# Kernel tuning notes

Measured on AMD Instinct MI355X. Metric: run time of the kernel, lower is better.

The kernel has to match this reference:

```python
import jax, jax.numpy as jnp
import numpy as np

B, T, V, E, Hd, NTAG = 16, 512, 32000, 100, 500, 32
PAD, SOS, EOS = 0, 1, 2
NEG = -10000.0


def _lstm_dir(xs, mask, Wih, Whh, b, h0, c0, reverse):
    # xs: [T,B,D]; mask: [T,B] bool. Packed-sequence semantics: at padded
    # steps the state is frozen and the output is zero (pad_packed fills 0).
    def step(carry, inp):
        h, c = carry
        x_t, m = inp
        g = x_t @ Wih.T + h @ Whh.T + b
        i, f, gg, o = jnp.split(g, 4, axis=-1)  # torch gate order i,f,g,o
        c_new = jax.nn.sigmoid(f) * c + jax.nn.sigmoid(i) * jnp.tanh(gg)
        h_new = jax.nn.sigmoid(o) * jnp.tanh(c_new)
        m_ = m[:, None]
        return (jnp.where(m_, h_new, h), jnp.where(m_, c_new, c)), jnp.where(m_, h_new, 0.0)
    _, ys = jax.lax.scan(step, (h0, c0), (xs, mask), reverse=reverse)
    return ys


def _forward(x, y0, embed_W, Wih0, Whh0, bih0, bhh0, Wih1, Whh1, bih1, bhh1, W_out, b_out, trans, h0, c0):
    maskb = x > 0                       # [B,T]
    maskf = maskb.astype(embed_W.dtype)
    mT = maskb.T                        # [T,B]
    xs = embed_W[x].transpose(1, 0, 2)  # [T,B,E]
    # layer 0 (bidirectional)
    f0 = _lstm_dir(xs, mT, Wih0[0], Whh0[0], bih0[0] + bhh0[0], h0[0], c0[0], False)
    b0 = _lstm_dir(xs, mT, Wih0[1], Whh0[1], bih0[1] + bhh0[1], h0[1], c0[1], True)
    l1 = jnp.concatenate([f0, b0], axis=-1)  # [T,B,1000]
    # layer 1 (dropout omitted: deterministic reference)
    f1 = _lstm_dir(l1, mT, Wih1[0], Whh1[0], bih1[0] + bhh1[0], h0[2], c0[2], False)
    b1 = _lstm_dir(l1, mT, Wih1[1], Whh1[1], bih1[1] + bhh1[1], h0[3], c0[3], True)
    hseq = jnp.concatenate([f1, b1], axis=-1).transpose(1, 0, 2)  # [B,T,1000]
    # emissions, masked exactly as in loss(): y = y * mask
    y = (hseq @ W_out.T + b_out) * maskf[:, :, None]  # [B,T,NTAG]
    # gold path score (crf_score_batch)
    y0e = jnp.concatenate([jnp.full((B, 1), SOS, y0.dtype), y0], axis=1)
    emit = jnp.take_along_axis(y, y0e[:, 1:, None], axis=2)[..., 0]
    tr = trans[y0e[:, 1:], y0e[:, :-1]] * maskf
    gold = jnp.sum(emit + tr, axis=1)  # [B]
    # log-partition (crf_forward_batch). Faithful to the original, including
    # the quirk that finished rows are overwritten with max_g score[b,g].
    init = jnp.full((B, NTAG), NEG, y.dtype).at[:, SOS].set(0.0)
    def step(score, inp):
        emit_t, m_t = inp  # [B,NTAG], [B]
        z = score[:, None, :] + trans[None, :, :] + emit_t[:, :, None]  # [B,F,G]
        new = jax.nn.logsumexp(z, axis=2)
        carry = jnp.broadcast_to(jnp.max(score, axis=1, keepdims=True), score.shape)
        return jnp.where(m_t[:, None], new, carry), None
    final, _ = jax.lax.scan(step, init, (y.transpose(1, 0, 2), mT))
    Z = jax.nn.logsumexp(final, axis=1)
    return jnp.mean(Z - gold)


def setup_inputs() -> dict:
    key = jax.random.key(0)
    ks = jax.random.split(key, 14)
    rng = np.random.default_rng(0)
    lengths = np.sort(rng.integers(T // 4, T + 1, size=B))[::-1]  # sorted desc (pack_padded)
    valid = np.arange(T)[None, :] < lengths[:, None]
    x = rng.integers(1, V, size=(B, T)) * valid
    y0 = rng.integers(3, NTAG, size=(B, T)) * valid
    rn = lambda k, s, sc=0.1: jax.random.normal(k, s, jnp.float32) * sc
    embed_W = rn(ks[0], (V, E)).at[0].set(0.0)  # padding_idx=0
    Wih0, Whh0 = rn(ks[1], (2, 4 * Hd, E)), rn(ks[2], (2, 4 * Hd, Hd))
    bih0, bhh0 = rn(ks[3], (2, 4 * Hd)), rn(ks[4], (2, 4 * Hd))
    Wih1, Whh1 = rn(ks[5], (2, 4 * Hd, 2 * Hd)), rn(ks[6], (2, 4 * Hd, Hd))
    bih1, bhh1 = rn(ks[7], (2, 4 * Hd)), rn(ks[8], (2, 4 * Hd))
    W_out, b_out = rn(ks[9], (NTAG, 2 * Hd)), rn(ks[10], (NTAG,))
    trans = jax.random.normal(ks[11], (NTAG, NTAG), jnp.float32)
    trans = trans.at[SOS, :].set(NEG).at[:, EOS].set(NEG).at[:, PAD].set(NEG).at[PAD, :].set(NEG)
    trans = trans.at[PAD, EOS].set(0.0).at[PAD, PAD].set(0.0)
    h0 = jax.random.normal(ks[12], (4, B, Hd), jnp.float32)
    c0 = jax.random.normal(ks[13], (4, B, Hd), jnp.float32)
    return dict(x=jnp.asarray(x, jnp.int32), y0=jnp.asarray(y0, jnp.int32), embed_W=embed_W,
                Wih0=Wih0, Whh0=Whh0, bih0=bih0, bhh0=bhh0, Wih1=Wih1, Whh1=Whh1,
                bih1=bih1, bhh1=bhh1, W_out=W_out, b_out=b_out, trans=trans, h0=h0, c0=c0)


def reference(x, y0, embed_W, Wih0, Whh0, bih0, bhh0, Wih1, Whh1, bih1, bhh1, W_out, b_out, trans, h0, c0):
    return _forward(x, y0, embed_W, Wih0, Whh0, bih0, bhh0, Wih1, Whh1, bih1, bhh1, W_out, b_out, trans, h0, c0)
```

## Files before the change

### kernel.cpp

```cpp
#include <hip/hip_runtime.h>
#include <hip/hip_fp16.h>
#include <math.h>

#define TT 512
#define BB 16
#define EE 100
#define HD 500
#define NEG (-10000.0f)
#define SENT64 0xFFFFFFFFFFFFFFFFull
#define SENT32 0xFFFFFFFFu

typedef __attribute__((ext_vector_type(8))) short short8;
typedef __attribute__((ext_vector_type(4))) float f32x4;
typedef __attribute__((ext_vector_type(4))) unsigned int u32x4;
typedef __attribute__((ext_vector_type(2))) unsigned int u32x2;

__device__ inline short f2bf(float f) {
    unsigned u = __builtin_bit_cast(unsigned, f);
    unsigned r = (u + 0x7fffu + ((u >> 16) & 1u)) >> 16;
    return (short)r;
}
__device__ inline unsigned short f2h(float f) {
    __half h = __float2half(f);
    return __builtin_bit_cast(unsigned short, h);
}
__device__ inline float h2f(unsigned short u) {
    __half h = __builtin_bit_cast(__half, u);
    return __half2float(h);
}
__device__ inline float bf2f(unsigned short u) {
    return __builtin_bit_cast(float, ((unsigned)u) << 16);
}
__device__ inline float sigm_fast(float x) {
    return __builtin_amdgcn_rcpf(1.f + __expf(-x));
}
__device__ inline float tanh_fast(float x) {
    return 1.f - 2.f * __builtin_amdgcn_rcpf(__expf(2.f * x) + 1.f);
}
__device__ inline void store_u16_wt(unsigned short* p, unsigned short v) {
    asm volatile("global_store_short %0, %1, off sc0 sc1" :: "v"(p), "v"((unsigned)v) : "memory");
}
__device__ inline void store_sent16(void* p) {
    u32x4 s = {SENT32, SENT32, SENT32, SENT32};
    asm volatile("global_store_dwordx4 %0, %1, off sc0 sc1" :: "v"(p), "v"(s) : "memory");
}

#define NSENTB   4104
#define NEMB     4096
#define NWC0     2000
#define NPAD     384
__global__ __launch_bounds__(256) void prep_kernel(
    const int* __restrict__ x, int* __restrict__ mlen,
    unsigned long long* __restrict__ sentp, int* __restrict__ gcnt,
    const float* __restrict__ EW, unsigned short* __restrict__ XS,
    const float* __restrict__ Wih0, unsigned short* __restrict__ Wb0,
    int* __restrict__ H0pad) {
    int bid = blockIdx.x;
    int tid = threadIdx.x;
    if (bid == 0) {
        __shared__ int mx;
        if (tid == 0) mx = 1;
        if (tid < 132)
            __hip_atomic_store(gcnt + tid, 0, __ATOMIC_RELAXED, __HIP_MEMORY_SCOPE_AGENT);
        __syncthreads();
        int any0 = 0, any1 = 0;
        for (int b = 0; b < BB; ++b) {
            any0 |= (x[b * TT + tid] > 0);
            any1 |= (x[b * TT + tid + 256] > 0);
        }
        if (any0) atomicMax(&mx, tid + 1);
        if (any1) atomicMax(&mx, tid + 257);
        __syncthreads();
        if (tid == 0) mlen[0] = mx;
        return;
    }
    bid -= 1;
    if (bid < NSENTB) {
        int i = bid * 256 + tid;
        store_sent16((char*)sentp + (size_t)i * 16);
        return;
    }
    bid -= NSENTB;
    if (bid < NEMB) {
        int idx = bid * 256 + tid;
        int e = idx & 127;
        int r = idx >> 7;
        int t = r >> 4;
        int b = r & 15;
        unsigned short v = 0;
        if (e < EE) {
            int tok = x[b * TT + t];
            v = (unsigned short)f2bf(EW[(size_t)tok * EE + e]);
        }
        XS[idx] = v;
        return;
    }
    bid -= NEMB;
    if (bid < NWC0) {
        int i = bid * 256 + tid;
        int r = i >> 7;
        int k = i & 127;
        int z = r / 2000;
        int rl = r - z * 2000;
        int logical = (rl & 3) * 500 + (rl >> 2);
        Wb0[i] = (k < 100)
            ? (unsigned short)f2bf(Wih0[((size_t)z * 2000 + logical) * 100 + k]) : 0;
        return;
    }
    bid -= NWC0;
    {
        int i = bid * 256 + tid;
        if (i < 8192 * 12) {
            int r = i / 12, c = i - r * 12;
            H0pad[r * 512 + 500 + c] = 0;
        }
    }
}

__global__ void sentfill_kernel(unsigned long long* __restrict__ p, int n16,
                                int* __restrict__ cnt) {
    int i = blockIdx.x * 256 + threadIdx.x;
    if (i < n16)
        store_sent16((char*)p + (size_t)i * 16);
    if (cnt && blockIdx.x == 0 && threadIdx.x < 132)
        __hip_atomic_store(cnt + threadIdx.x, 0, __ATOMIC_RELAXED, __HIP_MEMORY_SCOPE_AGENT);
}

__device__ __forceinline__ void gemm_body(
    const unsigned short* __restrict__ A, const unsigned short* __restrict__ W,
    const float* __restrict__ b1, const float* __restrict__ b2,
    unsigned short* __restrict__ C, int Kpad, int bx, int by, int z,
    int* gcnt) {
    __shared__ __align__(16) unsigned short AsS[128 * 40];
    __shared__ __align__(16) unsigned short WsS[64 * 40];
    const int tid = threadIdx.x;
    const int lane = tid & 63;
    const int w = tid >> 6;
    const int quad = lane >> 4;
    const int nl = lane & 15;
    const int bm0 = bx * 128;
    const int n0 = by * 64;

    const unsigned short* Wz = W + (size_t)z * 2000 * Kpad;
    unsigned short* Cz = C + (size_t)z * 8192 * 2000;
    const float* b1z = b1 + (size_t)z * 2000;
    const float* b2z = b2 + (size_t)z * 2000;

    f32x4 acc[2][4];
#pragma unroll
    for (int mt = 0; mt < 2; ++mt)
#pragma unroll
        for (int nt = 0; nt < 4; ++nt) acc[mt][nt] = (f32x4){0.f, 0.f, 0.f, 0.f};

    const int arow = tid >> 2;
    const int kc = tid & 3;
    const int wn = n0 + arow;
    const bool wok = (wn < 2000);

    const unsigned short* Ap0 = A + (size_t)(bm0 + arow) * Kpad + kc * 8;
    const unsigned short* Ap1 = A + (size_t)(bm0 + 64 + arow) * Kpad + kc * 8;
    const unsigned short* Wp  = Wz + (size_t)(wok ? wn : 0) * Kpad + kc * 8;

    short8 av0 = *(const short8*)(Ap0);
    short8 av1 = *(const short8*)(Ap1);
    short8 wv = {0, 0, 0, 0, 0, 0, 0, 0};
    if (wok) wv = *(const short8*)(Wp);

    for (int k0 = 0; k0 < Kpad; k0 += 32) {
        __syncthreads();
        *(short8*)&AsS[arow * 40 + kc * 8] = av0;
        *(short8*)&AsS[(64 + arow) * 40 + kc * 8] = av1;
        *(short8*)&WsS[arow * 40 + kc * 8] = wv;
        __syncthreads();

        if (k0 + 32 < Kpad) {
            av0 = *(const short8*)(Ap0 + k0 + 32);
            av1 = *(const short8*)(Ap1 + k0 + 32);
            if (wok) wv = *(const short8*)(Wp + k0 + 32);
        }

        short8 af[2], bfr[4];
#pragma unroll
        for (int mt = 0; mt < 2; ++mt)
            af[mt] = *(const short8*)&AsS[(w * 32 + mt * 16 + nl) * 40 + quad * 8];
#pragma unroll
        for (int nt = 0; nt < 4; ++nt)
            bfr[nt] = *(const short8*)&WsS[(nt * 16 + nl) * 40 + quad * 8];
#pragma unroll
        for (int mt = 0; mt < 2; ++mt)
#pragma unroll
            for (int nt = 0; nt < 4; ++nt)
                acc[mt][nt] = __builtin_amdgcn_mfma_f32_16x16x32_bf16(
                    af[mt], bfr[nt], acc[mt][nt], 0, 0, 0);
    }

#pragma unroll
    for (int nt = 0; nt < 4; ++nt) {
        int n = n0 + nt * 16 + nl;
        if (n < 2000) {
            int lg = n & 3, kk = n >> 2;
            float bb = b1z[lg * 500 + kk] + b2z[lg * 500 + kk];
#pragma unroll
            for (int mt = 0; mt < 2; ++mt) {
                int mbase = bm0 + w * 32 + mt * 16 + quad * 4;
#pragma unroll
                for (int reg = 0; reg < 4; ++reg)
                    store_u16_wt(&Cz[(size_t)(mbase + reg) * 2000 + n],
                                 f2h(acc[mt][nt][reg] + bb));
            }
        }
    }
    asm volatile("s_waitcnt vmcnt(0)" ::: "memory");
    __syncthreads();
    if (tid == 0)
        __hip_atomic_fetch_add(&gcnt[z * 64 + bx], 1,
                               __ATOMIC_RELAXED, __HIP_MEMORY_SCOPE_AGENT);
}

__device__ __forceinline__ void rec_body(
    const unsigned short* __restrict__ G, const float* __restrict__ Whh,
    const int* __restrict__ x, const float* __restrict__ h0,
    const float* __restrict__ c0, int layerbase,
    unsigned short* __restrict__ Hout, unsigned short* __restrict__ hseq,
    const int* __restrict__ mlen, int* gcnt, int blk)
{
    const int dir = blk >> 4;
    const int bsl = blk & 15;
    const int k0 = bsl * 32;
    const int tid = threadIdx.x;
    const int lane = tid & 63;
    const int w = tid >> 6;
    const int quad = lane >> 4;
    const int nl = lane & 15;
    const int L = mlen[0];

    const float* Wd = Whh + (size_t)dir * 2000 * HD;
    const unsigned short* Gd = G + (size_t)dir * TT * BB * 2000;
    unsigned short* hdir = hseq + (size_t)dir * (TT + 1) * 8192;

    __shared__ __align__(16) unsigned short hstage[8192];
    __shared__ float sg[4][32][17];

    short8 bf[2][16];
#pragma unroll
    for (int tl = 0; tl < 2; ++tl) {
        int tt = w * 2 + tl;
        int r = tt * 16 + nl;
        int g = r >> 5;
        int lkr = r & 31;
        int kk = k0 + lkr;
        const float* wrow = (kk < HD) ? (Wd + (size_t)(g * HD + kk) * HD) : (const float*)0;
#pragma unroll
        for (int ks = 0; ks < 16; ++ks) {
            int kg0 = ks * 32 + quad * 8;
            short8 v;
            if (wrow && kg0 + 8 <= HD) {
                float4 f0 = *(const float4*)(wrow + kg0);
                float4 f1 = *(const float4*)(wrow + kg0 + 4);
                v[0] = f2bf(f0.x); v[1] = f2bf(f0.y); v[2] = f2bf(f0.z); v[3] = f2bf(f0.w);
                v[4] = f2bf(f1.x); v[5] = f2bf(f1.y); v[6] = f2bf(f1.z); v[7] = f2bf(f1.w);
            } else {
#pragma unroll
                for (int j = 0; j < 8; ++j) {
                    int kg = kg0 + j;
                    float f = (wrow && kg < HD) ? wrow[kg] : 0.f;
                    v[j] = f2bf(f);
                }
            }
            bf[tl][ks] = v;
        }
    }

    const int lk = tid & 31;
    const int k  = k0 + lk;
    const bool kok = (k < HD);
    const int b0v = tid >> 5;
    const int b1v = 8 + (tid >> 5);
    float h_st[2] = {0.f, 0.f}, c_st[2] = {0.f, 0.f};
    if (kok) {
        size_t base0 = (size_t)(layerbase + dir) * BB * HD + (size_t)b0v * HD + k;
        size_t base1 = (size_t)(layerbase + dir) * BB * HD + (size_t)b1v * HD + k;
        h_st[0] = h0[base0]; c_st[0] = c0[base0];
        h_st[1] = h0[base1]; c_st[1] = c0[base1];
    }

    {
        int i0 = (int)(unsigned short)f2bf(kok ? h_st[0] : 0.f);
        int i1 = (int)(unsigned short)f2bf(kok ? h_st[1] : 0.f);
        int a0 = __shfl_down(i0, 1), c0s = __shfl_down(i0, 2), d0 = __shfl_down(i0, 3);
        int a1 = __shfl_down(i1, 1), c1s = __shfl_down(i1, 2), d1 = __shfl_down(i1, 3);
        if ((lk & 3) == 0) {
            unsigned long long p0 = (unsigned long long)(unsigned)(i0 | (a0 << 16))
                                  | ((unsigned long long)(unsigned)(c0s | (d0 << 16)) << 32);
            unsigned long long p1 = (unsigned long long)(unsigned)(i1 | (a1 << 16))
                                  | ((unsigned long long)(unsigned)(c1s | (d1 << 16)) << 32);
            int idx0 = bsl * 512 + (b0v + 16 * (lk >> 3)) * 8 + (lk & 7);
            int idx1 = bsl * 512 + (b1v + 16 * (lk >> 3)) * 8 + (lk & 7);
            __hip_atomic_store((unsigned long long*)(hdir + idx0), p0,
                               __ATOMIC_RELAXED, __HIP_MEMORY_SCOPE_AGENT);
            __hip_atomic_store((unsigned long long*)(hdir + idx1), p1,
                               __ATOMIC_RELAXED, __HIP_MEMORY_SCOPE_AGENT);
        }
    }

    u32x2 ga = {0, 0}, gb = {0, 0};
    int m[2]; m[0] = m[1] = 0;
    int lastTile = -1;

    {
        int t = dir ? (L - 1) : 0;
        if (gcnt) {
            int tile = dir * 64 + (t >> 3);
            while (__hip_atomic_load(&gcnt[tile], __ATOMIC_RELAXED,
                                     __HIP_MEMORY_SCOPE_AGENT) < 32) {}
            lastTile = tile;
        }
        if (kok) {
            const unsigned short* gr0 = Gd + ((size_t)t * BB + b0v) * 2000 + (size_t)k * 4;
            const unsigned short* gr1 = Gd + ((size_t)t * BB + b1v) * 2000 + (size_t)k * 4;
            asm volatile(
                "global_load_dwordx2 %0, %2, off sc0 sc1\n\t"
                "global_load_dwordx2 %1, %3, off sc0 sc1"
                : "=&v"(ga), "=&v"(gb) : "v"(gr0), "v"(gr1) : "memory");
            m[0] = x[b0v * TT + t] > 0;
            m[1] = x[b1v * TT + t] > 0;
        }
    }

    for (int s = 0; s < L; ++s) {
        const int t = dir ? (L - 1 - s) : s;
        const unsigned short* bufr = hdir + (size_t)s * 8192;
        unsigned short* bufw = hdir + (size_t)(s + 1) * 8192;

        {
            const unsigned short* p0 = bufr + (tid +   0) * 8;
            const unsigned short* p1 = bufr + (tid + 256) * 8;
            const unsigned short* p2 = bufr + (tid + 512) * 8;
            const unsigned short* p3 = bufr + (tid + 768) * 8;
            u32x4 c0v, c1v, c2v, c3v;
            for (;;) {
                asm volatile(
                    "global_load_dwordx4 %0, %6, off sc0 sc1\n\t"
                    "global_load_dwordx4 %1, %7, off sc0 sc1\n\t"
                    "global_load_dwordx4 %2, %8, off sc0 sc1\n\t"
                    "global_load_dwordx4 %3, %9, off sc0 sc1\n\t"
                    "s_waitcnt vmcnt(0)"
                    : "=&v"(c0v), "=&v"(c1v), "=&v"(c2v), "=&v"(c3v),
                      "+v"(ga), "+v"(gb)
                    : "v"(p0), "v"(p1), "v"(p2), "v"(p3)
                    : "memory");
                unsigned bad = 0;
#pragma unroll
                for (int q = 0; q < 4; ++q)
                    bad |= (c0v[q] == SENT32) | (c1v[q] == SENT32)
                         | (c2v[q] == SENT32) | (c3v[q] == SENT32);
                if (!bad) break;
            }
            *(u32x4*)&hstage[(tid +   0) * 8] = c0v;
            *(u32x4*)&hstage[(tid + 256) * 8] = c1v;
            *(u32x4*)&hstage[(tid + 512) * 8] = c2v;
            *(u32x4*)&hstage[(tid + 768) * 8] = c3v;
        }
        __syncthreads();

        f32x4 acc0 = {0.f, 0.f, 0.f, 0.f};
        f32x4 acc1 = {0.f, 0.f, 0.f, 0.f};
#pragma unroll
        for (int ks = 0; ks < 16; ++ks) {
            short8 a = *(const short8*)&hstage[ks * 512 + lane * 8];
            acc0 = __builtin_amdgcn_mfma_f32_16x16x32_bf16(a, bf[0][ks], acc0, 0, 0, 0);
            acc1 = __builtin_amdgcn_mfma_f32_16x16x32_bf16(a, bf[1][ks], acc1, 0, 0, 0);
        }

        {
            int r0 = (w * 2 + 0) * 16 + nl;
            int r1 = (w * 2 + 1) * 16 + nl;
            int g0r = r0 >> 5, lk0 = r0 & 31;
            int g1r = r1 >> 5, lk1 = r1 & 31;
#pragma unroll
            for (int reg = 0; reg < 4; ++reg) {
                int b = quad * 4 + reg;
                sg[g0r][lk0][b] = acc0[reg];
                sg[g1r][lk1][b] = acc1[reg];
            }
        }
        __syncthreads();

        int i0 = 0, i1 = 0;
        if (kok) {
            {
                unsigned w0 = ga[0], w1 = ga[1];
                float si  = sg[0][lk][b0v] + h2f((unsigned short)(w0 & 0xffffu));
                float sf  = sg[1][lk][b0v] + h2f((unsigned short)(w0 >> 16));
                float sgg = sg[2][lk][b0v] + h2f((unsigned short)(w1 & 0xffffu));
                float so  = sg[3][lk][b0v] + h2f((unsigned short)(w1 >> 16));
                float c_new = sigm_fast(sf) * c_st[0] + sigm_fast(si) * tanh_fast(sgg);
                float h_new = sigm_fast(so) * tanh_fast(c_new);
                if (m[0]) { h_st[0] = h_new; c_st[0] = c_new; }
            }
            {
                unsigned w0 = gb[0], w1 = gb[1];
                float si  = sg[0][lk][b1v] + h2f((unsigned short)(w0 & 0xffffu));
                float sf  = sg[1][lk][b1v] + h2f((unsigned short)(w0 >> 16));
                float sgg = sg[2][lk][b1v] + h2f((unsigned short)(w1 & 0xffffu));
                float so  = sg[3][lk][b1v] + h2f((unsigned short)(w1 >> 16));
                float c_new = sigm_fast(sf) * c_st[1] + sigm_fast(si) * tanh_fast(sgg);
                float h_new = sigm_fast(so) * tanh_fast(c_new);
                if (m[1]) { h_st[1] = h_new; c_st[1] = c_new; }
            }
            i0 = (int)(unsigned short)f2bf(h_st[0]);
            i1 = (int)(unsigned short)f2bf(h_st[1]);
        }

        {
            int a0 = __shfl_down(i0, 1), c0s = __shfl_down(i0, 2), d0 = __shfl_down(i0, 3);
            int a1 = __shfl_down(i1, 1), c1s = __shfl_down(i1, 2), d1 = __shfl_down(i1, 3);
            if ((lk & 3) == 0) {
                unsigned long long p0 = (unsigned long long)(unsigned)(i0 | (a0 << 16))
                                      | ((unsigned long long)(unsigned)(c0s | (d0 << 16)) << 32);
                unsigned long long p1 = (unsigned long long)(unsigned)(i1 | (a1 << 16))
                                      | ((unsigned long long)(unsigned)(c1s | (d1 << 16)) << 32);
                int idx0 = bsl * 512 + (b0v + 16 * (lk >> 3)) * 8 + (lk & 7);
                int idx1 = bsl * 512 + (b1v + 16 * (lk >> 3)) * 8 + (lk & 7);
                __hip_atomic_store((unsigned long long*)(bufw + idx0), p0,
                                   __ATOMIC_RELAXED, __HIP_MEMORY_SCOPE_AGENT);
                __hip_atomic_store((unsigned long long*)(bufw + idx1), p1,
                                   __ATOMIC_RELAXED, __HIP_MEMORY_SCOPE_AGENT);
            }
        }

        if (kok) {
            Hout[((size_t)t * BB + b0v) * 1024 + dir * HD + k] =
                (unsigned short)(m[0] ? i0 : 0);
            Hout[((size_t)t * BB + b1v) * 1024 + dir * HD + k] =
                (unsigned short)(m[1] ? i1 : 0);
        }

        if (s + 1 < L) {
            int tn = dir ? (L - 2 - s) : (s + 1);
            if (gcnt) {
                int tile = dir * 64 + (tn >> 3);
                if (tile != lastTile) {
                    while (__hip_atomic_load(&gcnt[tile], __ATOMIC_RELAXED,
                                             __HIP_MEMORY_SCOPE_AGENT) < 32) {}
                    lastTile = tile;
                }
            }
            if (kok) {
                const unsigned short* gr0 = Gd + ((size_t)tn * BB + b0v) * 2000 + (size_t)k * 4;
                const unsigned short* gr1 = Gd + ((size_t)tn * BB + b1v) * 2000 + (size_t)k * 4;
                asm volatile(
                    "global_load_dwordx2 %0, %2, off sc0 sc1\n\t"
                    "global_load_dwordx2 %1, %3, off sc0 sc1"
                    : "=&v"(ga), "=&v"(gb) : "v"(gr0), "v"(gr1) : "memory");
                m[0] = x[b0v * TT + tn] > 0;
                m[1] = x[b1v * TT + tn] > 0;
            }
        }
    }
}

__global__ __launch_bounds__(256, 1) void fused_kernel(
    const unsigned short* __restrict__ A, const unsigned short* __restrict__ Wb,
    const float* __restrict__ b1, const float* __restrict__ b2,
    unsigned short* __restrict__ Gh, int Kpad,
    const float* __restrict__ Whh, const int* __restrict__ x,
    const float* __restrict__ h0, const float* __restrict__ c0, int layerbase,
    unsigned short* __restrict__ Hout, unsigned short* __restrict__ hseq,
    const int* __restrict__ mlen, int* gcnt,
    const float* __restrict__ Wc_src, unsigned short* __restrict__ Wc_dst) {
    int bid = blockIdx.x;
    if (bid < 32) {
        rec_body(Gh, Whh, x, h0, c0, layerbase, Hout, hseq, mlen, gcnt, bid);
    } else if (bid < 32 + 4096) {
        int gx = bid - 32;
        int z = gx & 1;
        int rem = gx >> 1;
        int bx = rem >> 5;
        int by = rem & 31;
        if (z) bx = 63 - bx;
        gemm_body(A, Wb, b1, b2, Gh, Kpad, bx, by, z, gcnt);
    } else {
        int i = (bid - 4128) * 256 + threadIdx.x;
        int r = i >> 10;
        int k = i & 1023;
        int z = r / 2000;
        int rl = r - z * 2000;
        int logical = (rl & 3) * 500 + (rl >> 2);
        Wc_dst[i] = (k < 1000)
            ? (unsigned short)f2bf(Wc_src[((size_t)z * 2000 + logical) * 1000 + k]) : 0;
    }
}

__global__ __launch_bounds__(256) void outproj_kernel(
    const unsigned short* __restrict__ HS, const float* __restrict__ Wo,
    const float* __restrict__ bo, const int* __restrict__ x,
    float* __restrict__ Y) {
    __shared__ float wlds[8 * 1000];
    const int bid = blockIdx.x;
    const int tid = threadIdx.x;
    const int rblk = bid >> 2;
    const int n0 = (bid & 3) * 8;
    for (int i = tid; i < 8000; i += 256) {
        int nn = i / 1000;
        int q = i - nn * 1000;
        wlds[i] = Wo[(size_t)(n0 + nn) * 1000 + q];
    }
    __syncthreads();
    const int r = rblk * 32 + (tid >> 3);
    const int n = n0 + (tid & 7);
    const int t = r >> 4;
    const int b = r & 15;
    float out = 0.f;
    if (x[b * TT + t] > 0) {
        const unsigned short* h = HS + (size_t)r * 1024;
        const float* wrow = &wlds[(tid & 7) * 1000];
        float s = 0.f;
#pragma unroll 4
        for (int q = 0; q < 1000; q += 8) {
            short8 hv = *(const short8*)(h + q);
            float4 w0 = *(const float4*)(wrow + q);
            float4 w1 = *(const float4*)(wrow + q + 4);
            s += bf2f((unsigned short)hv[0]) * w0.x + bf2f((unsigned short)hv[1]) * w0.y
               + bf2f((unsigned short)hv[2]) * w0.z + bf2f((unsigned short)hv[3]) * w0.w
               + bf2f((unsigned short)hv[4]) * w1.x + bf2f((unsigned short)hv[5]) * w1.y
               + bf2f((unsigned short)hv[6]) * w1.z + bf2f((unsigned short)hv[7]) * w1.w;
        }
        out = s + bo[n];
    }
    Y[(size_t)r * 32 + n] = out;
}

__global__ __launch_bounds__(64) void crf_kernel(
    const float* __restrict__ Y, const int* __restrict__ x, const int* __restrict__ y0,
    const float* __restrict__ trans, float* __restrict__ out_pb,
    float* __restrict__ out, int* __restrict__ fcnt) {
    const int b = blockIdx.x;
    const int lane = threadIdx.x;
    const int i = lane & 31;
    const int half = lane >> 5;
    __shared__ float sc[32];

    float tr[16];
#pragma unroll
    for (int jj = 0; jj < 16; ++jj) tr[jj] = trans[i * 32 + half * 16 + jj];

    float gp = 0.f;
    for (int t = lane; t < TT; t += 64) {
        int xm = x[b * TT + t];
        float mf = (xm > 0) ? 1.f : 0.f;
        int ynext = y0[b * TT + t];
        int yprev = (t == 0) ? 1 : y0[b * TT + t - 1];
        gp += Y[((size_t)t * BB + b) * 32 + ynext] + trans[ynext * 32 + yprev] * mf;
    }
#pragma unroll
    for (int d = 32; d >= 1; d >>= 1) gp += __shfl_down(gp, d);
    float goldS = __shfl(gp, 0);

    if (half == 0) sc[i] = (i == 1) ? 0.f : NEG;

    float emit_c = Y[(size_t)b * 32 + i];
    int mm_c = x[b * TT + 0] > 0;
    for (int t = 0; t < TT; ++t) {
        float emit_n = 0.f;
        int mm_n = 0;
        if (t + 1 < TT) {
            emit_n = Y[((size_t)(t + 1) * BB + b) * 32 + i];
            mm_n = x[b * TT + t + 1] > 0;
        }
        const float* sch = &sc[half * 16];
        float4 s0 = *(const float4*)(sch + 0);
        float4 s1 = *(const float4*)(sch + 4);
        float4 s2 = *(const float4*)(sch + 8);
        float4 s3 = *(const float4*)(sch + 12);
        float sj[16] = {s0.x, s0.y, s0.z, s0.w, s1.x, s1.y, s1.z, s1.w,
                        s2.x, s2.y, s2.z, s2.w, s3.x, s3.y, s3.z, s3.w};
        if (mm_c) {
            float z[16];
#pragma unroll
            for (int jj = 0; jj < 16; ++jj) z[jj] = sj[jj] + tr[jj];
            float m1 = z[0];
#pragma unroll
            for (int jj = 1; jj < 16; ++jj) m1 = fmaxf(m1, z[jj]);
            float mx = fmaxf(m1, __shfl_xor(m1, 32));
            float e1 = 0.f;
#pragma unroll
            for (int jj = 0; jj < 16; ++jj) e1 += __expf(z[jj] - mx);
            float et = e1 + __shfl_xor(e1, 32);
            float newv = emit_c + mx + __logf(et);
            if (half == 0) sc[i] = newv;
        } else {
            float c1 = sj[0];
#pragma unroll
            for (int jj = 1; jj < 16; ++jj) c1 = fmaxf(c1, sj[jj]);
            float cm = fmaxf(c1, __shfl_xor(c1, 32));
            if (half == 0) sc[i] = cm;
            break;
        }
        emit_c = emit_n;
        mm_c = mm_n;
    }

    float v = sc[i];
    float mx = v;
#pragma unroll
    for (int d = 16; d >= 1; d >>= 1) mx = fmaxf(mx, __shfl_xor(mx, d));
    float e = __expf(v - mx);
#pragma unroll
    for (int d = 16; d >= 1; d >>= 1) e += __shfl_xor(e, d);

    if (lane == 0) {
        float zb = (mx + __logf(e)) - goldS;
        __hip_atomic_store(&out_pb[b], zb, __ATOMIC_RELAXED, __HIP_MEMORY_SCOPE_AGENT);
        asm volatile("s_waitcnt vmcnt(0)" ::: "memory");
        int old = __hip_atomic_fetch_add(fcnt, 1, __ATOMIC_RELAXED,
                                         __HIP_MEMORY_SCOPE_AGENT);
        if (old == BB - 1) {
            float s = 0.f;
            for (int bb = 0; bb < BB; ++bb)
                s += __hip_atomic_load(&out_pb[bb], __ATOMIC_RELAXED,
                                       __HIP_MEMORY_SCOPE_AGENT);
            out[0] = s / (float)BB;
        }
    }
}

extern "C" void kernel_launch(void* const* d_in, const int* in_sizes, int n_in,
                              void* d_out, int out_size, void* d_ws, size_t ws_size,
                              hipStream_t stream) {
    const int*   x     = (const int*)d_in[0];
    const int*   y0    = (const int*)d_in[1];
    const float* EW    = (const float*)d_in[2];
    const float* Wih0  = (const float*)d_in[3];
    const float* Whh0  = (const float*)d_in[4];
    const float* bih0  = (const float*)d_in[5];
    const float* bhh0  = (const float*)d_in[6];
    const float* Wih1  = (const float*)d_in[7];
    const float* Whh1  = (const float*)d_in[8];
    const float* bih1  = (const float*)d_in[9];
    const float* bhh1  = (const float*)d_in[10];
    const float* Wo    = (const float*)d_in[11];
    const float* bo    = (const float*)d_in[12];
    const float* trans = (const float*)d_in[13];
    const float* h0    = (const float*)d_in[14];
    const float* c0    = (const float*)d_in[15];

    float* ws = (float*)d_ws;
    unsigned short* XS = (unsigned short*)ws;
    float* Y      = ws;
    float* crfbuf = ws + 262144;
    unsigned short* Gh   = (unsigned short*)(ws + 524288);
    unsigned short* H0b  = (unsigned short*)(ws + 16908288);
    unsigned short* HSb  = (unsigned short*)(ws + 21102592);
    unsigned short* Wb0  = (unsigned short*)(ws + 25296896);
    unsigned short* Wb1  = (unsigned short*)(ws + 25552896);
    unsigned short* hseq = (unsigned short*)(ws + 27600896);
    int* mlen     = (int*)(ws + 31803392);
    int* gcnt     = (int*)(ws + 31803393);
    int* fcnt     = gcnt + 128;
    const int nsent16 = 2 * (TT + 1) * 8192 / 8;

    const int nprep = 1 + NSENTB + NEMB + NWC0 + NPAD;
    prep_kernel<<<nprep, 256, 0, stream>>>(x, mlen, (unsigned long long*)hseq, gcnt,
                                           EW, XS, Wih0, Wb0, (int*)H0b);

    fused_kernel<<<32 + 4096 + 16000, 256, 0, stream>>>(
        XS, Wb0, bih0, bhh0, Gh, 128, Whh0, x, h0, c0, 0, H0b, hseq, mlen, gcnt,
        Wih1, Wb1);

    sentfill_kernel<<<NSENTB, 256, 0, stream>>>((unsigned long long*)hseq, nsent16, gcnt);

    fused_kernel<<<32 + 4096, 256, 0, stream>>>(
        H0b, Wb1, bih1, bhh1, Gh, 1024, Whh1, x, h0, c0, 2, HSb, hseq, mlen, gcnt,
        nullptr, nullptr);

    outproj_kernel<<<1024, 256, 0, stream>>>(HSb, Wo, bo, x, Y);

    crf_kernel<<<BB, 64, 0, stream>>>(Y, x, y0, trans, crfbuf, (float*)d_out, fcnt);
}
```

Baseline: 2.393 ms.

## Move mlen and sentinel fill into fused layer-0 kernel; retile outproj; register CRF

The max-length computation and the hseq sentinel fill move out of the prep kernel and into the first fused kernel as extra blocks. Recurrence blocks spin on a prep counter before reading mlen, so this setup work can overlap the layer-0 input GEMM. The output projection now has each block handle 16 tags with vectorized weight loads and computes two outputs per thread. The CRF recursion keeps its score in a register and shares it with ds_bpermute instead of through LDS. The spin-wait relies on all the sentinel blocks getting scheduled while the recurrence blocks occupy CUs, which adds a risk of deadlock or stalls.

```diff
diff --git a/kernel.cpp b/kernel.cpp
--- a/kernel.cpp
+++ b/kernel.cpp
@@ -49,38 +49,21 @@
 #define NEMB     4096
 #define NWC0     2000
 #define NPAD     384
-__global__ __launch_bounds__(256) void prep_kernel(
-    const int* __restrict__ x, int* __restrict__ mlen,
-    unsigned long long* __restrict__ sentp, int* __restrict__ gcnt,
+#define PREPTGT  (NSENTB + 1)
+
+__global__ __launch_bounds__(256) void prep2_kernel(
+    const int* __restrict__ x, int* __restrict__ gcnt,
     const float* __restrict__ EW, unsigned short* __restrict__ XS,
     const float* __restrict__ Wih0, unsigned short* __restrict__ Wb0,
     int* __restrict__ H0pad) {
     int bid = blockIdx.x;
     int tid = threadIdx.x;
     if (bid == 0) {
-        __shared__ int mx;
-        if (tid == 0) mx = 1;
-        if (tid < 132)
+        if (tid < 136)
             __hip_atomic_store(gcnt + tid, 0, __ATOMIC_RELAXED, __HIP_MEMORY_SCOPE_AGENT);
-        __syncthreads();
-        int any0 = 0, any1 = 0;
-        for (int b = 0; b < BB; ++b) {
-            any0 |= (x[b * TT + tid] > 0);
-            any1 |= (x[b * TT + tid + 256] > 0);
-        }
-        if (any0) atomicMax(&mx, tid + 1);
-        if (any1) atomicMax(&mx, tid + 257);
-        __syncthreads();
-        if (tid == 0) mlen[0] = mx;
         return;
     }
     bid -= 1;
-    if (bid < NSENTB) {
-        int i = bid * 256 + tid;
-        store_sent16((char*)sentp + (size_t)i * 16);
-        return;
-    }
-    bid -= NSENTB;
     if (bid < NEMB) {
         int idx = bid * 256 + tid;
         int e = idx & 127;
@@ -222,7 +205,7 @@
     const int* __restrict__ x, const float* __restrict__ h0,
     const float* __restrict__ c0, int layerbase,
     unsigned short* __restrict__ Hout, unsigned short* __restrict__ hseq,
-    const int* __restrict__ mlen, int* gcnt, int blk)
+    int* __restrict__ mlen, int* gcnt, int* prepcnt, int blk)
 {
     const int dir = blk >> 4;
     const int bsl = blk & 15;
@@ -232,7 +215,6 @@
     const int w = tid >> 6;
     const int quad = lane >> 4;
     const int nl = lane & 15;
-    const int L = mlen[0];
 
     const float* Wd = Whh + (size_t)dir * 2000 * HD;
     const unsigned short* Gd = G + (size_t)dir * TT * BB * 2000;
@@ -282,6 +264,18 @@
         size_t base1 = (size_t)(layerbase + dir) * BB * HD + (size_t)b1v * HD + k;
         h_st[0] = h0[base0]; c_st[0] = c0[base0];
         h_st[1] = h0[base1]; c_st[1] = c0[base1];
+    }
+
+    int L;
+    if (prepcnt) {
+        if (tid == 0) {
+            while (__hip_atomic_load(prepcnt, __ATOMIC_ACQUIRE,
+                                     __HIP_MEMORY_SCOPE_AGENT) < PREPTGT) {}
+        }
+        __syncthreads();
+        L = __hip_atomic_load(mlen, __ATOMIC_RELAXED, __HIP_MEMORY_SCOPE_AGENT);
+    } else {
+        L = mlen[0];
     }
 
     {
@@ -467,13 +461,53 @@
     const float* __restrict__ Whh, const int* __restrict__ x,
     const float* __restrict__ h0, const float* __restrict__ c0, int layerbase,
     unsigned short* __restrict__ Hout, unsigned short* __restrict__ hseq,
-    const int* __restrict__ mlen, int* gcnt,
-    const float* __restrict__ Wc_src, unsigned short* __restrict__ Wc_dst) {
+    int* __restrict__ mlen, int* gcnt,
+    const float* __restrict__ Wc_src, unsigned short* __restrict__ Wc_dst,
+    int* prepcnt) {
     int bid = blockIdx.x;
+    int tid = threadIdx.x;
+    if (prepcnt == nullptr) {
+        if (bid < 32) {
+            rec_body(Gh, Whh, x, h0, c0, layerbase, Hout, hseq, mlen, gcnt, nullptr, bid);
+        } else {
+            int gx = bid - 32;
+            int z = gx & 1;
+            int rem = gx >> 1;
+            int bx = rem >> 5;
+            int by = rem & 31;
+            if (z) bx = 63 - bx;
+            gemm_body(A, Wb, b1, b2, Gh, Kpad, bx, by, z, gcnt);
+        }
+        return;
+    }
     if (bid < 32) {
-        rec_body(Gh, Whh, x, h0, c0, layerbase, Hout, hseq, mlen, gcnt, bid);
-    } else if (bid < 32 + 4096) {
-        int gx = bid - 32;
+        rec_body(Gh, Whh, x, h0, c0, layerbase, Hout, hseq, mlen, gcnt, prepcnt, bid);
+    } else if (bid == 32) {
+        __shared__ int mx;
+        if (tid == 0) mx = 1;
+        __syncthreads();
+        int any0 = 0, any1 = 0;
+        for (int b = 0; b < BB; ++b) {
+            any0 |= (x[b * TT + tid] > 0);
+            any1 |= (x[b * TT + tid + 256] > 0);
+        }
+        if (any0) atomicMax(&mx, tid + 1);
+        if (any1) atomicMax(&mx, tid + 257);
+        __syncthreads();
+        if (tid == 0) {
+            __hip_atomic_store(mlen, mx, __ATOMIC_RELAXED, __HIP_MEMORY_SCOPE_AGENT);
+            asm volatile("s_waitcnt vmcnt(0)" ::: "memory");
+            __hip_atomic_fetch_add(prepcnt, 1, __ATOMIC_RELEASE, __HIP_MEMORY_SCOPE_AGENT);
+        }
+    } else if (bid < 33 + NSENTB) {
+        int i = (bid - 33) * 256 + tid;
+        store_sent16((char*)hseq + (size_t)i * 16);
+        asm volatile("s_waitcnt vmcnt(0)" ::: "memory");
+        __syncthreads();
+        if (tid == 0)
+            __hip_atomic_fetch_add(prepcnt, 1, __ATOMIC_RELEASE, __HIP_MEMORY_SCOPE_AGENT);
+    } else if (bid < 4137 + 4096) {
+        int gx = bid - 4137;
         int z = gx & 1;
         int rem = gx >> 1;
         int bx = rem >> 5;
@@ -481,7 +515,7 @@
         if (z) bx = 63 - bx;
         gemm_body(A, Wb, b1, b2, Gh, Kpad, bx, by, z, gcnt);
     } else {
-        int i = (bid - 4128) * 256 + threadIdx.x;
+        int i = (bid - 8233) * 256 + tid;
         int r = i >> 10;
         int k = i & 1023;
         int z = r / 2000;
@@ -496,39 +530,46 @@
     const unsigned short* __restrict__ HS, const float* __restrict__ Wo,
     const float* __restrict__ bo, const int* __restrict__ x,
     float* __restrict__ Y) {
-    __shared__ float wlds[8 * 1000];
+    __shared__ float wlds[16 * 1000];
     const int bid = blockIdx.x;
     const int tid = threadIdx.x;
-    const int rblk = bid >> 2;
-    const int n0 = (bid & 3) * 8;
-    for (int i = tid; i < 8000; i += 256) {
-        int nn = i / 1000;
-        int q = i - nn * 1000;
-        wlds[i] = Wo[(size_t)(n0 + nn) * 1000 + q];
-    }
+    const int rblk = bid >> 1;
+    const int nh = (bid & 1) * 16;
+    for (int i = tid * 4; i < 16000; i += 1024)
+        *(float4*)&wlds[i] = *(const float4*)&Wo[(size_t)nh * 1000 + i];
     __syncthreads();
     const int r = rblk * 32 + (tid >> 3);
-    const int n = n0 + (tid & 7);
+    const int na = nh + (tid & 7) * 2;
+    const int nb = na + 1;
     const int t = r >> 4;
     const int b = r & 15;
-    float out = 0.f;
+    float outa = 0.f, outb = 0.f;
     if (x[b * TT + t] > 0) {
         const unsigned short* h = HS + (size_t)r * 1024;
-        const float* wrow = &wlds[(tid & 7) * 1000];
-        float s = 0.f;
+        const float* wa = &wlds[(tid & 7) * 2 * 1000];
+        const float* wb = wa + 1000;
+        float sa = 0.f, sb = 0.f;
 #pragma unroll 4
         for (int q = 0; q < 1000; q += 8) {
             short8 hv = *(const short8*)(h + q);
-            float4 w0 = *(const float4*)(wrow + q);
-            float4 w1 = *(const float4*)(wrow + q + 4);
-            s += bf2f((unsigned short)hv[0]) * w0.x + bf2f((unsigned short)hv[1]) * w0.y
-               + bf2f((unsigned short)hv[2]) * w0.z + bf2f((unsigned short)hv[3]) * w0.w
-               + bf2f((unsigned short)hv[4]) * w1.x + bf2f((unsigned short)hv[5]) * w1.y
-               + bf2f((unsigned short)hv[6]) * w1.z + bf2f((unsigned short)hv[7]) * w1.w;
-        }
-        out = s + bo[n];
-    }
-    Y[(size_t)r * 32 + n] = out;
+            float h0f = bf2f((unsigned short)hv[0]), h1f = bf2f((unsigned short)hv[1]);
+            float h2 = bf2f((unsigned short)hv[2]), h3 = bf2f((unsigned short)hv[3]);
+            float h4 = bf2f((unsigned short)hv[4]), h5 = bf2f((unsigned short)hv[5]);
+            float h6 = bf2f((unsigned short)hv[6]), h7 = bf2f((unsigned short)hv[7]);
+            float4 a0 = *(const float4*)(wa + q);
+            float4 a1 = *(const float4*)(wa + q + 4);
+            float4 b0 = *(const float4*)(wb + q);
+            float4 b1 = *(const float4*)(wb + q + 4);
+            sa += h0f * a0.x + h1f * a0.y + h2 * a0.z + h3 * a0.w
+                + h4 * a1.x + h5 * a1.y + h6 * a1.z + h7 * a1.w;
+            sb += h0f * b0.x + h1f * b0.y + h2 * b0.z + h3 * b0.w
+                + h4 * b1.x + h5 * b1.y + h6 * b1.z + h7 * b1.w;
+        }
+        outa = sa + bo[na];
+        outb = sb + bo[nb];
+    }
+    Y[(size_t)r * 32 + na] = outa;
+    Y[(size_t)r * 32 + nb] = outb;
 }
 
 __global__ __launch_bounds__(64) void crf_kernel(
@@ -539,11 +580,14 @@
     const int lane = threadIdx.x;
     const int i = lane & 31;
     const int half = lane >> 5;
-    __shared__ float sc[32];
 
     float tr[16];
-#pragma unroll
-    for (int jj = 0; jj < 16; ++jj) tr[jj] = trans[i * 32 + half * 16 + jj];
+    int baddr[16];
+#pragma unroll
+    for (int jj = 0; jj < 16; ++jj) {
+        tr[jj] = trans[i * 32 + half * 16 + jj];
+        baddr[jj] = (half * 16 + jj) * 4;
+    }
 
     float gp = 0.f;
     for (int t = lane; t < TT; t += 64) {
@@ -557,7 +601,7 @@
     for (int d = 32; d >= 1; d >>= 1) gp += __shfl_down(gp, d);
     float goldS = __shfl(gp, 0);
 
-    if (half == 0) sc[i] = (i == 1) ? 0.f : NEG;
+    float sc_reg = (i == 1) ? 0.f : NEG;
 
     float emit_c = Y[(size_t)b * 32 + i];
     int mm_c = x[b * TT + 0] > 0;
@@ -568,13 +612,12 @@
             emit_n = Y[((size_t)(t + 1) * BB + b) * 32 + i];
             mm_n = x[b * TT + t + 1] > 0;
         }
-        const float* sch = &sc[half * 16];
-        float4 s0 = *(const float4*)(sch + 0);
-        float4 s1 = *(const float4*)(sch + 4);
-        float4 s2 = *(const float4*)(sch + 8);
-        float4 s3 = *(const float4*)(sch + 12);
-        float sj[16] = {s0.x, s0.y, s0.z, s0.w, s1.x, s1.y, s1.z, s1.w,
-                        s2.x, s2.y, s2.z, s2.w, s3.x, s3.y, s3.z, s3.w};
+        float sj[16];
+        int scbits = __builtin_bit_cast(int, sc_reg);
+#pragma unroll
+        for (int jj = 0; jj < 16; ++jj)
+            sj[jj] = __builtin_bit_cast(float,
+                        __builtin_amdgcn_ds_bpermute(baddr[jj], scbits));
         if (mm_c) {
             float z[16];
 #pragma unroll
@@ -587,21 +630,19 @@
 #pragma unroll
             for (int jj = 0; jj < 16; ++jj) e1 += __expf(z[jj] - mx);
             float et = e1 + __shfl_xor(e1, 32);
-            float newv = emit_c + mx + __logf(et);
-            if (half == 0) sc[i] = newv;
+            sc_reg = emit_c + mx + __logf(et);
         } else {
             float c1 = sj[0];
 #pragma unroll
             for (int jj = 1; jj < 16; ++jj) c1 = fmaxf(c1, sj[jj]);
-            float cm = fmaxf(c1, __shfl_xor(c1, 32));
-            if (half == 0) sc[i] = cm;
+            sc_reg = fmaxf(c1, __shfl_xor(c1, 32));
             break;
         }
         emit_c = emit_n;
         mm_c = mm_n;
     }
 
-    float v = sc[i];
+    float v = sc_reg;
     float mx = v;
 #pragma unroll
     for (int d = 16; d >= 1; d >>= 1) mx = fmaxf(mx, __shfl_xor(mx, d));
@@ -658,23 +699,23 @@
     int* mlen     = (int*)(ws + 31803392);
     int* gcnt     = (int*)(ws + 31803393);
     int* fcnt     = gcnt + 128;
+    int* prepcnt  = gcnt + 132;
     const int nsent16 = 2 * (TT + 1) * 8192 / 8;
 
-    const int nprep = 1 + NSENTB + NEMB + NWC0 + NPAD;
-    prep_kernel<<<nprep, 256, 0, stream>>>(x, mlen, (unsigned long long*)hseq, gcnt,
-                                           EW, XS, Wih0, Wb0, (int*)H0b);
-
-    fused_kernel<<<32 + 4096 + 16000, 256, 0, stream>>>(
+    const int nprep2 = 1 + NEMB + NWC0 + NPAD;
+    prep2_kernel<<<nprep2, 256, 0, stream>>>(x, gcnt, EW, XS, Wih0, Wb0, (int*)H0b);
+
+    fused_kernel<<<32 + 1 + NSENTB + 4096 + 16000, 256, 0, stream>>>(
         XS, Wb0, bih0, bhh0, Gh, 128, Whh0, x, h0, c0, 0, H0b, hseq, mlen, gcnt,
-        Wih1, Wb1);
+        Wih1, Wb1, prepcnt);
 
     sentfill_kernel<<<NSENTB, 256, 0, stream>>>((unsigned long long*)hseq, nsent16, gcnt);
 
     fused_kernel<<<32 + 4096, 256, 0, stream>>>(
         H0b, Wb1, bih1, bhh1, Gh, 1024, Whh1, x, h0, c0, 2, HSb, hseq, mlen, gcnt,
-        nullptr, nullptr);
-
-    outproj_kernel<<<1024, 256, 0, stream>>>(HSb, Wo, bo, x, Y);
+        nullptr, nullptr, nullptr);
+
+    outproj_kernel<<<512, 256, 0, stream>>>(HSb, Wo, bo, x, Y);
 
     crf_kernel<<<BB, 64, 0, stream>>>(Y, x, y0, trans, crfbuf, (float*)d_out, fcnt);
 }
```

New measurement: 2.462 ms. 2.9% more time.
